# Optimization experiments

Hardware: AMD Instinct MI355X
Metric: run time of the kernel (lower is better)

## Reference

```python
import jax, jax.numpy as jnp
import numpy as np

N = 256  # image box size
B, P, L = 32, 300000, 64


def _gauss_kernel(sigma=1.0, size=5):
    ax = np.arange(size) - size // 2
    g = np.exp(-(ax ** 2) / (2.0 * sigma ** 2))
    k = np.outer(g, g)
    k = k / k.sum()
    return jnp.asarray(k, jnp.float32)


def _splat(cx, cy, w):
    # bilinear scatter-splat of P weighted points into [B, N, N] images
    x0 = jnp.floor(cx)
    y0 = jnp.floor(cy)
    fx = cx - x0
    fy = cy - y0
    xi0 = jnp.clip(x0.astype(jnp.int32), 0, N - 1)
    yi0 = jnp.clip(y0.astype(jnp.int32), 0, N - 1)
    xi1 = jnp.clip(xi0 + 1, 0, N - 1)
    yi1 = jnp.clip(yi0 + 1, 0, N - 1)
    b = jnp.broadcast_to(jnp.arange(cx.shape[0])[:, None], cx.shape)
    img = jnp.zeros((cx.shape[0], N, N), cx.dtype)
    img = img.at[b, yi0, xi0].add(w * (1 - fx) * (1 - fy))
    img = img.at[b, yi0, xi1].add(w * fx * (1 - fy))
    img = img.at[b, yi1, xi0].add(w * (1 - fx) * fy)
    img = img.at[b, yi1, xi1].add(w * fx * fy)
    return img


def setup_inputs() -> dict:
    key = jax.random.key(0)
    ks = jax.random.split(key, 9)
    z_x = jax.random.normal(ks[0], (B, L), jnp.float32)
    z_y = jax.random.normal(ks[1], (B, L), jnp.float32)
    z_z = jax.random.normal(ks[2], (B, L), jnp.float32)
    # Zernike basis scaled so deformations are a few pixels
    Z = 0.05 * jax.random.normal(ks[3], (P, L), jnp.float32)
    # masked volume point coordinates, centered, within +-N/4
    coords = (jax.random.uniform(ks[4], (P, 3), jnp.float32) - 0.5) * (0.5 * N)
    weights = jax.random.uniform(ks[5], (P,), jnp.float32)
    # proper per-image rotation matrices from random Euler angles (zyz)
    rng = np.random.RandomState(0)
    ang = rng.uniform(-np.pi, np.pi, (B, 3))
    ca, sa = np.cos(ang), np.sin(ang)
    Rm = np.zeros((B, 3, 3), np.float32)
    for i in range(B):
        a, b2, g = ang[i]
        Rz1 = np.array([[np.cos(a), -np.sin(a), 0], [np.sin(a), np.cos(a), 0], [0, 0, 1]])
        Ry = np.array([[np.cos(b2), 0, np.sin(b2)], [0, 1, 0], [-np.sin(b2), 0, np.cos(b2)]])
        Rz2 = np.array([[np.cos(g), -np.sin(g), 0], [np.sin(g), np.cos(g), 0], [0, 0, 1]])
        Rm[i] = (Rz1 @ Ry @ Rz2).astype(np.float32)
    R = jnp.asarray(Rm)
    shifts = 5.0 * jax.random.normal(ks[6], (B, 2), jnp.float32)
    # per-image radial CTF filter in Fourier space
    f = np.fft.fftfreq(N).astype(np.float32)
    r2 = f[:, None] ** 2 + f[None, :] ** 2  # [N, N]
    df = rng.uniform(500.0, 1500.0, (B, 1, 1)).astype(np.float32)
    ctf = jnp.asarray(np.sin(np.pi * df * r2[None]), jnp.float32)
    return {"z_x": z_x, "z_y": z_y, "z_z": z_z, "Z": Z, "coords": coords,
            "weights": weights, "R": R, "shifts": shifts, "ctf": ctf}


def reference(z_x, z_y, z_z, Z, coords, weights, R, shifts, ctf):
    # computeDeformationField: d = z @ Z^T -> [B, P]
    d_x = z_x @ Z.T
    d_y = z_y @ Z.T
    d_z = z_z @ Z.T
    # applyDeformationField: add reference coordinates per axis
    c_x = coords[:, 0][None, :] + d_x
    c_y = coords[:, 1][None, :] + d_y
    c_z = coords[:, 2][None, :] + d_z
    # applyAlignmentMatrix: per-image rotation, keep projected x/y rows
    c_r_x = R[:, 0, 0:1] * c_x + R[:, 0, 1:2] * c_y + R[:, 0, 2:3] * c_z
    c_r_y = R[:, 1, 0:1] * c_x + R[:, 1, 1:2] * c_y + R[:, 1, 2:3] * c_z
    # applyShifts: per-image shift + box-center offset
    half = jnp.float32(N / 2)
    px = c_r_x + shifts[:, 0:1] + half
    py = c_r_y + shifts[:, 1:2] + half
    # scatterImgByPass: bilinear scatter splat
    w = jnp.broadcast_to(weights[None, :], px.shape)
    img = _splat(px, py, w)  # [B, N, N]
    # gaussianFilterImage: 5x5 Gaussian blur
    k = _gauss_kernel()
    img_f = jax.lax.conv_general_dilated(
        img[:, None], k[None, None], (1, 1), 'SAME',
        dimension_numbers=('NCHW', 'OIHW', 'NCHW'))[:, 0]
    # ctfFilterImage: FFT multiply by real CTF, inverse FFT
    ft = jnp.fft.fft2(img_f)
    out = jnp.real(jnp.fft.ifft2(ft * ctf.astype(ft.dtype)))
    return out
```

## Files before the change

kernel.cpp:

```cpp
#include <hip/hip_runtime.h>
#include <hip/hip_bf16.h>

#define NIMG 32
#define NPTS 300000
#define NL   64
#define NBOX 256

#define BANDS  4
#define BROWS  64
#define CHUNKS 2
#define CHPTS  (NPTS / CHUNKS)

#define WQS  2047.0f
#define WQI  (1.0f / 2047.0f)

typedef float v2f __attribute__((ext_vector_type(2)));
typedef float f32x4 __attribute__((ext_vector_type(4)));
typedef short bf16x8 __attribute__((ext_vector_type(8)));
typedef unsigned long long u64;

__device__ __forceinline__ int rev8(int x) { return (int)(__brev((unsigned)x) >> 24); }

__device__ __forceinline__ short f2bf(float f) {
    unsigned u = __float_as_uint(f);
    unsigned r = (u + 0x7FFFu + ((u >> 16) & 1u)) >> 16;
    return (short)r;
}

__global__ __launch_bounds__(256) void zero_kernel(float4* p, int n4) {
    int i = blockIdx.x * 256 + threadIdx.x;
    if (i < n4) p[i] = make_float4(0.f, 0.f, 0.f, 0.f);
}

__global__ __launch_bounds__(256) void uvprep_kernel(
    const float* __restrict__ z_x, const float* __restrict__ z_y,
    const float* __restrict__ z_z, const float* __restrict__ R,
    const float* __restrict__ shifts,
    float4* __restrict__ hdrbuf, short* __restrict__ Bt)
{
    __shared__ float s_u[NIMG * NL];
    __shared__ float s_v[NIMG * NL];
    int t = threadIdx.x;
    for (int e = t; e < NIMG * NL; e += 256) {
        int b = e >> 6;
        const float* Rb = R + b * 9;
        float zx = z_x[e], zy = z_y[e], zz = z_z[e];
        s_u[e] = Rb[0] * zx + Rb[1] * zy + Rb[2] * zz;
        s_v[e] = Rb[3] * zx + Rb[4] * zy + Rb[5] * zz;
    }
    if (t < NIMG) {
        const float* Rb = R + t * 9;
        hdrbuf[2 * t]     = make_float4(Rb[0], Rb[1], Rb[2], shifts[2 * t]     + 128.f);
        hdrbuf[2 * t + 1] = make_float4(Rb[3], Rb[4], Rb[5], shifts[2 * t + 1] + 128.f);
    }
    __syncthreads();
    for (int e = t; e < 64 * NL; e += 256) {
        int c = e >> 6, k = e & 63;
        int b = c >> 1;
        float val = (c & 1) ? s_v[b * NL + k] : s_u[b * NL + k];
        Bt[e] = f2bf(val);
    }
}

__device__ __forceinline__ u64 make_rec(float px, float py, float w) {
    float x0f = floorf(px), y0f = floorf(py);
    float fx = px - x0f, fy = py - y0f;
    int xi0 = min(max((int)x0f, 0), NBOX - 1);
    int yi0 = min(max((int)y0f, 0), NBOX - 1);
    float w00 = w * (1.f - fx) * (1.f - fy);
    float w10 = w * fx * (1.f - fy);
    float w01 = w * (1.f - fx) * fy;
    float w11 = w * fx * fy;
    if (xi0 == NBOX - 1) {
        w00 += w10; w10 = 0.f;
        w01 += w11; w11 = 0.f;
    }
    if (yi0 == NBOX - 1) {
        w00 += w01; w01 = 0.f;
        w10 += w11; w11 = 0.f;
    }
    return (u64)(unsigned)(xi0 | (yi0 << 8))
         | ((u64)(unsigned)(w00 * WQS + 0.5f) << 16)
         | ((u64)(unsigned)(w10 * WQS + 0.5f) << 28)
         | ((u64)(unsigned)(w01 * WQS + 0.5f) << 40)
         | ((u64)(unsigned)(w11 * WQS + 0.5f) << 52);
}

__global__ __launch_bounds__(256) void project_mfma_kernel(
    const float* __restrict__ Zb, const float* __restrict__ coords,
    const float* __restrict__ weights,
    const float4* __restrict__ hdrbuf, const short* __restrict__ Bt,
    u64* __restrict__ recs)
{
    int tid = threadIdx.x;
    int lane = tid & 63;
    int rg = (lane >> 4) & 3;
    bool oddl = (lane & 1);

    bf16x8 bf[4][2];
    #pragma unroll
    for (int t = 0; t < 4; ++t)
        #pragma unroll
        for (int q = 0; q < 2; ++q)
            bf[t][q] = *(const bf16x8*)(Bt + (t * 16 + (lane & 15)) * NL + q * 32 + rg * 8);

    int wid = blockIdx.x * 4 + (tid >> 6);
    int nw  = gridDim.x * 4;
    for (int mt = wid; mt < NPTS / 16; mt += nw) {
        int pbase = mt * 16;
        const float* zrow = Zb + (size_t)(pbase + (lane & 15)) * NL;
        bf16x8 a[2];
        #pragma unroll
        for (int q = 0; q < 2; ++q) {
            float4 f0 = *(const float4*)(zrow + q * 32 + rg * 8);
            float4 f1 = *(const float4*)(zrow + q * 32 + rg * 8 + 4);
            bf16x8 av;
            av[0] = f2bf(f0.x); av[1] = f2bf(f0.y); av[2] = f2bf(f0.z); av[3] = f2bf(f0.w);
            av[4] = f2bf(f1.x); av[5] = f2bf(f1.y); av[6] = f2bf(f1.z); av[7] = f2bf(f1.w);
            a[q] = av;
        }
        f32x4 accs[4];
        #pragma unroll
        for (int t = 0; t < 4; ++t) {
            f32x4 acc = {0.f, 0.f, 0.f, 0.f};
            acc = __builtin_amdgcn_mfma_f32_16x16x32_bf16(a[0], bf[t][0], acc, 0, 0, 0);
            acc = __builtin_amdgcn_mfma_f32_16x16x32_bf16(a[1], bf[t][1], acc, 0, 0, 0);
            accs[t] = acc;
        }

        int ra = rg * 4 + (oddl ? 2 : 0);
        int pa = pbase + ra;
        float cax = coords[3 * pa],     cay = coords[3 * pa + 1], caz = coords[3 * pa + 2];
        float cbx = coords[3 * pa + 3], cby = coords[3 * pa + 4], cbz = coords[3 * pa + 5];
        float wa = weights[pa], wb = weights[pa + 1];

        #pragma unroll
        for (int t = 0; t < 4; ++t) {
            f32x4 acc = accs[t];
            float o0 = __shfl_xor(acc[0], 1, 64);
            float o1 = __shfl_xor(acc[1], 1, 64);
            float o2 = __shfl_xor(acc[2], 1, 64);
            float o3 = __shfl_xor(acc[3], 1, 64);
            float m0 = oddl ? acc[2] : acc[0];
            float m1 = oddl ? acc[3] : acc[1];
            float t0 = oddl ? o2 : o0;
            float t1 = oddl ? o3 : o1;
            float dxa = oddl ? t0 : m0;
            float dya = oddl ? m0 : t0;
            float dxb = oddl ? t1 : m1;
            float dyb = oddl ? m1 : t1;
            int col = t * 16 + (lane & 15);
            int img = col >> 1;
            float4 h0 = hdrbuf[2 * img], h1 = hdrbuf[2 * img + 1];
            float affxa = fmaf(h0.x, cax, fmaf(h0.y, cay, fmaf(h0.z, caz, h0.w)));
            float affya = fmaf(h1.x, cax, fmaf(h1.y, cay, fmaf(h1.z, caz, h1.w)));
            float affxb = fmaf(h0.x, cbx, fmaf(h0.y, cby, fmaf(h0.z, cbz, h0.w)));
            float affyb = fmaf(h1.x, cbx, fmaf(h1.y, cby, fmaf(h1.z, cbz, h1.w)));
            u64* pb = recs + (size_t)img * NPTS;
            pb[pa]     = make_rec(affxa + dxa, affya + dya, wa);
            pb[pa + 1] = make_rec(affxb + dxb, affyb + dyb, wb);
        }
    }
}

__global__ __launch_bounds__(1024) void splat2_kernel(
    const u64* __restrict__ recs, float* __restrict__ img)
{
    __shared__ u64 VA[32 * 128];
    __shared__ u64 VB[32 * 129];
    __shared__ u64 VC[32 * 128];
    __shared__ u64 VD[32 * 129];
    int tid = threadIdx.x;
    int id = blockIdx.x;
    int band = id >> 6;
    int g    = id & 63;
    int b = g >> 1, c = g & 1;

    for (int i = tid; i < 32 * 128; i += 1024) { VA[i] = 0ULL; VC[i] = 0ULL; }
    for (int i = tid; i < 32 * 129; i += 1024) { VB[i] = 0ULL; VD[i] = 0ULL; }
    __syncthreads();

    const int y_lo = band * BROWS;
    const u64* rp = recs + (size_t)b * NPTS + (size_t)c * CHPTS;

    for (int i = 4 * tid; i < CHPTS; i += 4096) {
        ulonglong2 R01 = *(const ulonglong2*)(rp + i);
        ulonglong2 R23 = *(const ulonglong2*)(rp + i + 2);
        u64 Ra[4] = {R01.x, R01.y, R23.x, R23.y};
        #pragma unroll
        for (int k = 0; k < 4; ++k) {
            u64 rec = Ra[k];
            unsigned ps = (unsigned)rec & 0xFFFFu;
            int xi0 = ps & 255;
            int yi0 = ps >> 8;
            int r0 = yi0 - y_lo;
            if ((unsigned)r0 >= BROWS) continue;
            u64 val = ((rec >> 16) & 0xFFFULL)
                    | (((rec >> 28) & 0xFFFULL) << 16)
                    | (((rec >> 40) & 0xFFFULL) << 32)
                    | (((rec >> 52) & 0xFFFULL) << 48);
            int qr = r0 >> 1;
            int qc = (xi0 + (xi0 & 1)) >> 1;
            bool xodd = (xi0 & 1), yodd = (r0 & 1);
            u64* base = yodd ? (xodd ? VD : VC) : (xodd ? VB : VA);
            int stride = xodd ? 129 : 128;
            atomicAdd(&base[qr * stride + qc], val);
        }
    }
    __syncthreads();
    int nrows = min(BROWS + 1, NBOX - y_lo);
    float* ib = img + (size_t)b * NBOX * NBOX + (size_t)y_lo * NBOX;
    for (int i = tid; i < nrows * NBOX; i += 1024) {
        int r = i >> 8, x = i & 255;
        int fc0 = x & 1;
        int fc1 = fc0 ^ 1;
        int ja = x >> 1;
        int jb = (x + 1) >> 1;
        unsigned acc = 0;
        if (r < BROWS) {
            int fr = (r & 1) << 1;
            acc += (unsigned)((VA[(r >> 1) * 128 + ja] >> (16 * (fr | fc0))) & 0xFFFFu);
            acc += (unsigned)((VB[(r >> 1) * 129 + jb] >> (16 * (fr | fc1))) & 0xFFFFu);
        }
        if (r >= 1) {
            int fr = ((r & 1) ^ 1) << 1;
            acc += (unsigned)((VC[((r - 1) >> 1) * 128 + ja] >> (16 * (fr | fc0))) & 0xFFFFu);
            acc += (unsigned)((VD[((r - 1) >> 1) * 129 + jb] >> (16 * (fr | fc1))) & 0xFFFFu);
        }
        if (acc) unsafeAtomicAdd(ib + i, (float)acc * WQI);
    }
}

__global__ __launch_bounds__(256) void splat_kernel(
    const float* __restrict__ z_x, const float* __restrict__ z_y,
    const float* __restrict__ z_z, const float* __restrict__ Zb,
    const float* __restrict__ coords, const float* __restrict__ weights,
    const float* __restrict__ R, const float* __restrict__ shifts,
    float* __restrict__ img)
{
    __shared__ float s_z[3][NIMG][NL];
    __shared__ float s_R[NIMG][9];
    __shared__ float s_sh[NIMG][2];

    int tid = threadIdx.x;
    for (int i = tid; i < NIMG * NL; i += 256) {
        (&s_z[0][0][0])[i] = z_x[i];
        (&s_z[1][0][0])[i] = z_y[i];
        (&s_z[2][0][0])[i] = z_z[i];
    }
    for (int i = tid; i < NIMG * 9; i += 256) (&s_R[0][0])[i] = R[i];
    if (tid < NIMG * 2) (&s_sh[0][0])[tid] = shifts[tid];
    __syncthreads();

    int p = blockIdx.x * 256 + tid;
    if (p >= NPTS) return;

    float4 zr[16];
    const float4* Zr4 = (const float4*)(Zb + (size_t)p * NL);
    #pragma unroll
    for (int i = 0; i < 16; ++i) zr[i] = Zr4[i];

    float cx0 = coords[3 * p + 0];
    float cy0 = coords[3 * p + 1];
    float cz0 = coords[3 * p + 2];
    float w   = weights[p];

    for (int b = 0; b < NIMG; ++b) {
        const float4* zx4 = (const float4*)s_z[0][b];
        const float4* zy4 = (const float4*)s_z[1][b];
        const float4* zz4 = (const float4*)s_z[2][b];
        float dx = 0.f, dy = 0.f, dz = 0.f;
        #pragma unroll
        for (int i = 0; i < 16; ++i) {
            float4 a = zx4[i];
            dx += a.x * zr[i].x + a.y * zr[i].y + a.z * zr[i].z + a.w * zr[i].w;
            float4 bb = zy4[i];
            dy += bb.x * zr[i].x + bb.y * zr[i].y + bb.z * zr[i].z + bb.w * zr[i].w;
            float4 c = zz4[i];
            dz += c.x * zr[i].x + c.y * zr[i].y + c.z * zr[i].z + c.w * zr[i].w;
        }
        float cx = cx0 + dx, cy = cy0 + dy, cz = cz0 + dz;
        const float* Rb = s_R[b];
        float px = Rb[0] * cx + Rb[1] * cy + Rb[2] * cz + s_sh[b][0] + 128.0f;
        float py = Rb[3] * cx + Rb[4] * cy + Rb[5] * cz + s_sh[b][1] + 128.0f;

        float x0 = floorf(px), y0 = floorf(py);
        float fx = px - x0, fy = py - y0;
        int xi0 = min(max((int)x0, 0), NBOX - 1);
        int yi0 = min(max((int)y0, 0), NBOX - 1);
        int xi1 = min(xi0 + 1, NBOX - 1);
        int yi1 = min(yi0 + 1, NBOX - 1);

        float* ib = img + (size_t)b * NBOX * NBOX;
        unsafeAtomicAdd(ib + yi0 * NBOX + xi0, w * (1.f - fx) * (1.f - fy));
        unsafeAtomicAdd(ib + yi0 * NBOX + xi1, w * fx * (1.f - fy));
        unsafeAtomicAdd(ib + yi1 * NBOX + xi0, w * (1.f - fx) * fy);
        unsafeAtomicAdd(ib + yi1 * NBOX + xi1, w * fx * fy);
    }
}

__device__ __forceinline__ void fft_dif_t(float2* s, const float2* tw, int t) {
    #pragma unroll
    for (int st = 7; st >= 0; --st) {
        int half = 1 << st;
        int j  = t & (half - 1);
        int i1 = ((t >> st) << (st + 1)) + j;
        int i2 = i1 + half;
        float2 a = s[i1], b = s[i2];
        float2 w = tw[j << (7 - st)];
        float dxr = a.x - b.x, dxi = a.y - b.y;
        s[i1] = make_float2(a.x + b.x, a.y + b.y);
        s[i2] = make_float2(w.x * dxr - w.y * dxi, w.x * dxi + w.y * dxr);
        __syncthreads();
    }
}

__device__ __forceinline__ void fft_dit_t(float2* s, const float2* tw, int t) {
    #pragma unroll
    for (int st = 0; st < 8; ++st) {
        int half = 1 << st;
        int j  = t & (half - 1);
        int i1 = ((t >> st) << (st + 1)) + j;
        int i2 = i1 + half;
        float2 a = s[i1], b = s[i2];
        float2 w = tw[j << (7 - st)];
        float cs = w.x, sn = -w.y;
        float tr = cs * b.x - sn * b.y;
        float ti = cs * b.y + sn * b.x;
        s[i1] = make_float2(a.x + tr, a.y + ti);
        s[i2] = make_float2(a.x - tr, a.y - ti);
        __syncthreads();
    }
}

__device__ __forceinline__ void init_tw(float2* tw, int tid) {
    if (tid < 128) {
        float sn, cs;
        sincosf(-6.283185307179586f * (float)tid * (1.0f / 256.0f), &sn, &cs);
        tw[tid] = make_float2(cs, sn);
    }
}

__global__ __launch_bounds__(256) void fft_rows_fwd_blur_kernel(const float* __restrict__ img,
                                                                float2* __restrict__ freq)
{
    __shared__ float2 s[2][NBOX];
    __shared__ float  sb[2][NBOX];
    __shared__ float2 tw[128];
    int tid = threadIdx.x;
    int tx = tid & 127, ty = tid >> 7;
    init_tw(tw, tid);
    int row = blockIdx.x * 2 + ty;
    int b = row >> 8, y = row & (NBOX - 1);
    const float* ib = img + ((size_t)b << 16);
    const float gw[5] = {0.0544886845f, 0.2442013420f, 0.4026199469f,
                         0.2442013420f, 0.0544886845f};
    float acc0 = 0.f, acc1 = 0.f;
    #pragma unroll
    for (int dy = -2; dy <= 2; ++dy) {
        int yy = y + dy;
        if ((unsigned)yy < (unsigned)NBOX) {
            const float* rp = ib + yy * NBOX;
            acc0 += gw[dy + 2] * rp[tx];
            acc1 += gw[dy + 2] * rp[tx + 128];
        }
    }
    sb[ty][tx] = acc0;  sb[ty][tx + 128] = acc1;
    __syncthreads();
    float r0 = 0.f, r1 = 0.f;
    #pragma unroll
    for (int dx = -2; dx <= 2; ++dx) {
        int x0 = tx + dx, x1 = tx + 128 + dx;
        if ((unsigned)x0 < (unsigned)NBOX) r0 += gw[dx + 2] * sb[ty][x0];
        if ((unsigned)x1 < (unsigned)NBOX) r1 += gw[dx + 2] * sb[ty][x1];
    }
    s[ty][tx]       = make_float2(r0, 0.f);
    s[ty][tx + 128] = make_float2(r1, 0.f);
    __syncthreads();
    fft_dif_t(s[ty], tw, tx);
    float2* op = freq + (size_t)row * NBOX;
    op[tx]       = s[ty][tx];
    op[tx + 128] = s[ty][tx + 128];
}

__global__ __launch_bounds__(1024) void fft_cols_ctf32_kernel(float2* __restrict__ freq,
                                                              const float* __restrict__ ctf)
{
    __shared__ float  s_re[32][257];
    __shared__ float  s_im[32][257];
    __shared__ float2 tw[128];
    int tid = threadIdx.x;
    init_tw(tw, tid);
    int col = tid & 31, tq = tid >> 5;
    int blk = blockIdx.x;
    int b = blk >> 3;
    int x = ((blk & 7) << 5) + col;
    float2* base = freq + ((size_t)b << 16) + x;

    #pragma unroll
    for (int k = 0; k < 8; ++k) {
        int j = tq + 32 * k;
        float2 v = base[(size_t)j * NBOX];
        s_re[col][j] = v.x;  s_im[col][j] = v.y;
    }
    __syncthreads();

    #pragma unroll
    for (int st = 7; st >= 0; --st) {
        int half = 1 << st;
        #pragma unroll
        for (int k = 0; k < 4; ++k) {
            int t = tq + 32 * k;
            int jj = t & (half - 1);
            int i1 = ((t >> st) << (st + 1)) + jj;
            int i2 = i1 + half;
            float ar = s_re[col][i1], ai = s_im[col][i1];
            float br = s_re[col][i2], bi = s_im[col][i2];
            float2 w = tw[jj << (7 - st)];
            float dr = ar - br, di = ai - bi;
            s_re[col][i1] = ar + br;  s_im[col][i1] = ai + bi;
            s_re[col][i2] = w.x * dr - w.y * di;
            s_im[col][i2] = w.x * di + w.y * dr;
        }
        __syncthreads();
    }

    const float* cb = ctf + ((size_t)b << 16) + rev8(x);
    #pragma unroll
    for (int k = 0; k < 8; ++k) {
        int j = tq + 32 * k;
        float c = cb[rev8(j) * NBOX];
        s_re[col][j] *= c;  s_im[col][j] *= c;
    }
    __syncthreads();

    #pragma unroll
    for (int st = 0; st < 8; ++st) {
        int half = 1 << st;
        #pragma unroll
        for (int k = 0; k < 4; ++k) {
            int t = tq + 32 * k;
            int jj = t & (half - 1);
            int i1 = ((t >> st) << (st + 1)) + jj;
            int i2 = i1 + half;
            float ar = s_re[col][i1], ai = s_im[col][i1];
            float br = s_re[col][i2], bi = s_im[col][i2];
            float2 w = tw[jj << (7 - st)];
            float cs = w.x, sn = -w.y;
            float tr = cs * br - sn * bi;
            float ti = cs * bi + sn * br;
            s_re[col][i1] = ar + tr;  s_im[col][i1] = ai + ti;
            s_re[col][i2] = ar - tr;  s_im[col][i2] = ai - ti;
        }
        __syncthreads();
    }

    const float inv = 1.0f / 256.0f;
    #pragma unroll
    for (int k = 0; k < 8; ++k) {
        int j = tq + 32 * k;
        base[(size_t)j * NBOX] = make_float2(s_re[col][j] * inv, s_im[col][j] * inv);
    }
}

__global__ __launch_bounds__(256) void fft_rows_inv_kernel(const float2* __restrict__ freq,
                                                           float* __restrict__ out)
{
    __shared__ float2 s[2][NBOX];
    __shared__ float2 tw[128];
    int tid = threadIdx.x;
    int tx = tid & 127, ty = tid >> 7;
    init_tw(tw, tid);
    int row = blockIdx.x * 2 + ty;
    const float2* rp = freq + (size_t)row * NBOX;
    s[ty][tx]       = rp[tx];
    s[ty][tx + 128] = rp[tx + 128];
    __syncthreads();
    fft_dit_t(s[ty], tw, tx);
    const float inv = 1.0f / 256.0f;
    out[(size_t)row * NBOX + tx]       = s[ty][tx].x * inv;
    out[(size_t)row * NBOX + tx + 128] = s[ty][tx + 128].x * inv;
}

extern "C" void kernel_launch(void* const* d_in, const int* in_sizes, int n_in,
                              void* d_out, int out_size, void* d_ws, size_t ws_size,
                              hipStream_t stream)
{
    (void)in_sizes; (void)n_in; (void)out_size;
    const float* z_x     = (const float*)d_in[0];
    const float* z_y     = (const float*)d_in[1];
    const float* z_z     = (const float*)d_in[2];
    const float* Zb      = (const float*)d_in[3];
    const float* coords  = (const float*)d_in[4];
    const float* weights = (const float*)d_in[5];
    const float* R       = (const float*)d_in[6];
    const float* shifts  = (const float*)d_in[7];
    const float* ctf     = (const float*)d_in[8];
    float* out = (float*)d_out;

    const size_t NELEM = (size_t)NIMG * NBOX * NBOX;
    char* base = (char*)d_ws;
    float* img  = (float*)base;
    u64*   recs = (u64*)(base + 8388608);
    float4* hdrbuf = (float4*)(base + 8388608 + 76800000);
    short*  Bt     = (short*)(base + 8388608 + 76800000 + 1024);
    float2* freq = (float2*)(base + 8388608);
    const size_t required = 8388608 + 76800000 + 1024 + 8192;

    zero_kernel<<<(int)(NELEM / 4 + 255) / 256, 256, 0, stream>>>((float4*)img, (int)(NELEM / 4));

    if (ws_size >= required) {
        uvprep_kernel<<<1, 256, 0, stream>>>(z_x, z_y, z_z, R, shifts, hdrbuf, Bt);
        project_mfma_kernel<<<2048, 256, 0, stream>>>(Zb, coords, weights,
                                                      hdrbuf, Bt, recs);
        splat2_kernel<<<NIMG * BANDS * CHUNKS, 1024, 0, stream>>>(recs, img);
    } else {
        splat_kernel<<<(NPTS + 255) / 256, 256, 0, stream>>>(z_x, z_y, z_z, Zb, coords,
                                                             weights, R, shifts, img);
    }

    fft_rows_fwd_blur_kernel<<<NIMG * NBOX / 2, 256, 0, stream>>>(img, freq);
    fft_cols_ctf32_kernel<<<NIMG * 8, 1024, 0, stream>>>(freq, ctf);
    fft_rows_inv_kernel<<<NIMG * NBOX / 2, 256, 0, stream>>>(freq, out);
}
```

Before: 140.1 us.

## Shrink per-point splat records to 32 bits and rebuild weights in splat kernel

The projection kernel now writes a 32-bit record per point per image holding the pixel index and 8-bit quantised fractional offsets, instead of a 64-bit record with four 12-bit corner weights. The splat kernel reads the shared per-point weight array and recomputes the four bilinear corner weights before the LDS atomics. This halves the intermediate record buffer written once and read four times (once per band), at the cost of extra arithmetic in the splat loop and coarser 8-bit quantisation of the fractional positions.

Result: no change. 138.1 us (median of 2 runs) (-1.5%).

```diff
diff --git a/kernel.cpp b/kernel.cpp
--- a/kernel.cpp
+++ b/kernel.cpp
@@ -62,35 +62,22 @@
     }
 }
 
-__device__ __forceinline__ u64 make_rec(float px, float py, float w) {
+__device__ __forceinline__ unsigned make_rec32(float px, float py) {
     float x0f = floorf(px), y0f = floorf(py);
     float fx = px - x0f, fy = py - y0f;
     int xi0 = min(max((int)x0f, 0), NBOX - 1);
     int yi0 = min(max((int)y0f, 0), NBOX - 1);
-    float w00 = w * (1.f - fx) * (1.f - fy);
-    float w10 = w * fx * (1.f - fy);
-    float w01 = w * (1.f - fx) * fy;
-    float w11 = w * fx * fy;
-    if (xi0 == NBOX - 1) {
-        w00 += w10; w10 = 0.f;
-        w01 += w11; w11 = 0.f;
-    }
-    if (yi0 == NBOX - 1) {
-        w00 += w01; w01 = 0.f;
-        w10 += w11; w11 = 0.f;
-    }
-    return (u64)(unsigned)(xi0 | (yi0 << 8))
-         | ((u64)(unsigned)(w00 * WQS + 0.5f) << 16)
-         | ((u64)(unsigned)(w10 * WQS + 0.5f) << 28)
-         | ((u64)(unsigned)(w01 * WQS + 0.5f) << 40)
-         | ((u64)(unsigned)(w11 * WQS + 0.5f) << 52);
+    unsigned fxq = (unsigned)(fx * 255.f + 0.5f); if (fxq > 255u) fxq = 255u;
+    unsigned fyq = (unsigned)(fy * 255.f + 0.5f); if (fyq > 255u) fyq = 255u;
+    if (xi0 == NBOX - 1) fxq = 0u;
+    if (yi0 == NBOX - 1) fyq = 0u;
+    return (unsigned)xi0 | ((unsigned)yi0 << 8) | (fxq << 16) | (fyq << 24);
 }
 
 __global__ __launch_bounds__(256) void project_mfma_kernel(
     const float* __restrict__ Zb, const float* __restrict__ coords,
-    const float* __restrict__ weights,
     const float4* __restrict__ hdrbuf, const short* __restrict__ Bt,
-    u64* __restrict__ recs)
+    unsigned* __restrict__ recs)
 {
     int tid = threadIdx.x;
     int lane = tid & 63;
@@ -132,7 +119,6 @@
         int pa = pbase + ra;
         float cax = coords[3 * pa],     cay = coords[3 * pa + 1], caz = coords[3 * pa + 2];
         float cbx = coords[3 * pa + 3], cby = coords[3 * pa + 4], cbz = coords[3 * pa + 5];
-        float wa = weights[pa], wb = weights[pa + 1];
 
         #pragma unroll
         for (int t = 0; t < 4; ++t) {
@@ -156,15 +142,17 @@
             float affya = fmaf(h1.x, cax, fmaf(h1.y, cay, fmaf(h1.z, caz, h1.w)));
             float affxb = fmaf(h0.x, cbx, fmaf(h0.y, cby, fmaf(h0.z, cbz, h0.w)));
             float affyb = fmaf(h1.x, cbx, fmaf(h1.y, cby, fmaf(h1.z, cbz, h1.w)));
-            u64* pb = recs + (size_t)img * NPTS;
-            pb[pa]     = make_rec(affxa + dxa, affya + dya, wa);
-            pb[pa + 1] = make_rec(affxb + dxb, affyb + dyb, wb);
+            unsigned r0_ = make_rec32(affxa + dxa, affya + dya);
+            unsigned r1_ = make_rec32(affxb + dxb, affyb + dyb);
+            unsigned* pb = recs + (size_t)img * NPTS;
+            *(u64*)(pb + pa) = (u64)r0_ | ((u64)r1_ << 32);
         }
     }
 }
 
 __global__ __launch_bounds__(1024) void splat2_kernel(
-    const u64* __restrict__ recs, float* __restrict__ img)
+    const unsigned* __restrict__ recs, const float* __restrict__ weights,
+    float* __restrict__ img)
 {
     __shared__ u64 VA[32 * 128];
     __shared__ u64 VB[32 * 129];
@@ -181,24 +169,32 @@
     __syncthreads();
 
     const int y_lo = band * BROWS;
-    const u64* rp = recs + (size_t)b * NPTS + (size_t)c * CHPTS;
+    const unsigned* rp = recs + (size_t)b * NPTS + (size_t)c * CHPTS;
+    const float*    wp = weights + (size_t)c * CHPTS;
 
     for (int i = 4 * tid; i < CHPTS; i += 4096) {
-        ulonglong2 R01 = *(const ulonglong2*)(rp + i);
-        ulonglong2 R23 = *(const ulonglong2*)(rp + i + 2);
-        u64 Ra[4] = {R01.x, R01.y, R23.x, R23.y};
+        uint4  Rv = *(const uint4*)(rp + i);
+        float4 Wv = *(const float4*)(wp + i);
+        unsigned Ra[4] = {Rv.x, Rv.y, Rv.z, Rv.w};
+        float    Wa[4] = {Wv.x, Wv.y, Wv.z, Wv.w};
         #pragma unroll
         for (int k = 0; k < 4; ++k) {
-            u64 rec = Ra[k];
-            unsigned ps = (unsigned)rec & 0xFFFFu;
-            int xi0 = ps & 255;
-            int yi0 = ps >> 8;
+            unsigned rec = Ra[k];
+            int xi0 = rec & 255;
+            int yi0 = (rec >> 8) & 255;
             int r0 = yi0 - y_lo;
             if ((unsigned)r0 >= BROWS) continue;
-            u64 val = ((rec >> 16) & 0xFFFULL)
-                    | (((rec >> 28) & 0xFFFULL) << 16)
-                    | (((rec >> 40) & 0xFFFULL) << 32)
-                    | (((rec >> 52) & 0xFFFULL) << 48);
+            float w  = Wa[k];
+            float fx = (float)((rec >> 16) & 255u) * (1.0f / 255.0f);
+            float fy = (float)(rec >> 24) * (1.0f / 255.0f);
+            float t1 = w * fy, t0 = w - t1;
+            float w10 = t0 * fx, w00 = t0 - w10;
+            float w11 = t1 * fx, w01 = t1 - w11;
+            unsigned q00 = (unsigned)(w00 * WQS + 0.5f);
+            unsigned q10 = (unsigned)(w10 * WQS + 0.5f);
+            unsigned q01 = (unsigned)(w01 * WQS + 0.5f);
+            unsigned q11 = (unsigned)(w11 * WQS + 0.5f);
+            u64 val = (u64)q00 | ((u64)q10 << 16) | ((u64)q01 << 32) | ((u64)q11 << 48);
             int qr = r0 >> 1;
             int qc = (xi0 + (xi0 & 1)) >> 1;
             bool xodd = (xi0 & 1), yodd = (r0 & 1);
@@ -500,20 +496,19 @@
 
     const size_t NELEM = (size_t)NIMG * NBOX * NBOX;
     char* base = (char*)d_ws;
-    float* img  = (float*)base;
-    u64*   recs = (u64*)(base + 8388608);
-    float4* hdrbuf = (float4*)(base + 8388608 + 76800000);
-    short*  Bt     = (short*)(base + 8388608 + 76800000 + 1024);
+    float*    img  = (float*)base;
+    unsigned* recs = (unsigned*)(base + 8388608);
+    float4* hdrbuf = (float4*)(base + 8388608 + 38400000);
+    short*  Bt     = (short*)(base + 8388608 + 38400000 + 1024);
     float2* freq = (float2*)(base + 8388608);
-    const size_t required = 8388608 + 76800000 + 1024 + 8192;
+    const size_t required = 8388608 + 38400000 + 1024 + 8192;
 
     zero_kernel<<<(int)(NELEM / 4 + 255) / 256, 256, 0, stream>>>((float4*)img, (int)(NELEM / 4));
 
     if (ws_size >= required) {
         uvprep_kernel<<<1, 256, 0, stream>>>(z_x, z_y, z_z, R, shifts, hdrbuf, Bt);
-        project_mfma_kernel<<<2048, 256, 0, stream>>>(Zb, coords, weights,
-                                                      hdrbuf, Bt, recs);
-        splat2_kernel<<<NIMG * BANDS * CHUNKS, 1024, 0, stream>>>(recs, img);
+        project_mfma_kernel<<<2048, 256, 0, stream>>>(Zb, coords, hdrbuf, Bt, recs);
+        splat2_kernel<<<NIMG * BANDS * CHUNKS, 1024, 0, stream>>>(recs, weights, img);
     } else {
         splat_kernel<<<(NPTS + 255) / 256, 256, 0, stream>>>(z_x, z_y, z_z, Zb, coords,
                                                              weights, R, shifts, img);
```
